# Optimization experiments

Hardware: AMD Instinct MI355X
Metric: run time of the kernel (lower is better)

## Reference

```python
import jax, jax.numpy as jnp
import numpy as np

N, E, IN, H, O = 50000, 800000, 256, 8, 32


def setup_inputs() -> dict:
    key = jax.random.key(0)
    ks = jax.random.split(key, 8)
    feat = jax.random.normal(ks[0], (N, IN), dtype=jnp.float32)
    src = jax.random.randint(ks[1], (E,), 0, N, dtype=jnp.int32)
    dst = jax.random.randint(ks[2], (E,), 0, N, dtype=jnp.int32)
    # Xavier-normal-ish parameter init
    W = jax.random.normal(ks[3], (IN, H * O), dtype=jnp.float32) * (2.0 / (IN + H * O)) ** 0.5
    attn_l = jax.random.normal(ks[4], (H, O), dtype=jnp.float32) * (2.0 / (1 + H * O)) ** 0.5
    attn_r = jax.random.normal(ks[5], (H, O), dtype=jnp.float32) * (2.0 / (1 + H * O)) ** 0.5
    bias = jnp.zeros((H * O,), dtype=jnp.float32)
    return {"feat": feat, "W": W, "attn_l": attn_l, "attn_r": attn_r, "bias": bias, "src": src, "dst": dst}


def reference(feat, W, attn_l, attn_r, bias, src, dst):
    # Linear projection: [N, IN] @ [IN, H*O] -> [N, H, O]
    ft = (feat @ W).reshape(-1, H, O)
    # Additive attention logits per node, per head
    el = jnp.einsum('nho,ho->nh', ft, attn_l)  # [N, H]
    er = jnp.einsum('nho,ho->nh', ft, attn_r)  # [N, H]
    # Edge-wise: e = leaky_relu(el[u] + er[v])
    e = jax.nn.leaky_relu(el[src] + er[dst], negative_slope=0.2)  # [E, H]
    # Segment softmax over incoming edges of each destination node
    emax = jax.ops.segment_max(e, dst, num_segments=N)            # [N, H]
    ee = jnp.exp(e - emax[dst])                                   # [E, H]
    denom = jax.ops.segment_sum(ee, dst, num_segments=N)          # [N, H]
    a = ee / denom[dst]                                           # [E, H]
    # Weighted scatter-sum aggregation: sum_u a_{uv} * ft_u
    msg = ft[src] * a[:, :, None]                                 # [E, H, O]
    rst = jax.ops.segment_sum(msg, dst, num_segments=N)           # [N, H, O]
    rst = rst + bias.reshape(1, H, O)
    return rst
```

## Files before the change

### kernel.cpp

```cpp
#include <hip/hip_runtime.h>

#define N_NODES 50000
#define N_EDGES 800000
#define NPAD    50176
#define SPILL_CAP 8192
#define GEMM_BLOCKS 782
#define BUCKET_BLOCKS 1563

typedef __bf16 bf16x8 __attribute__((ext_vector_type(8)));
typedef float  fx4    __attribute__((ext_vector_type(4)));
typedef unsigned short us8 __attribute__((ext_vector_type(8)));

__device__ __forceinline__ float b2f(unsigned short u) {
    return __uint_as_float(((unsigned)u) << 16);
}
__device__ __forceinline__ unsigned short f2b(float f) {
    unsigned x = __float_as_uint(f);
    return (unsigned short)((x + 0x7FFFu + ((x >> 16) & 1u)) >> 16);
}

__global__ __launch_bounds__(256) void prep_w(
    const float* __restrict__ W,
    unsigned short* __restrict__ Wt,
    int* __restrict__ cursor, int* __restrict__ spill_n) {
    __shared__ float T[64 * 65];
    int b = blockIdx.x, t = threadIdx.x;
    if (b < 16) {
        int bi = b >> 2, bj = b & 3;
        int r = t >> 2, cq = t & 3;
        const float* wp = W + (size_t)(bi * 64 + r) * 256 + bj * 64 + cq * 16;
#pragma unroll
        for (int i = 0; i < 16; ++i) T[r * 65 + cq * 16 + i] = wp[i];
        __syncthreads();
        int n = t >> 2, ks = (t & 3) * 16;
        us8 o0, o1;
#pragma unroll
        for (int i = 0; i < 8; ++i) o0[i] = f2b(T[(ks + i) * 65 + n]);
#pragma unroll
        for (int i = 0; i < 8; ++i) o1[i] = f2b(T[(ks + 8 + i) * 65 + n]);
        unsigned short* op = Wt + (size_t)(bj * 64 + n) * 256 + bi * 64 + ks;
        *reinterpret_cast<us8*>(op) = o0;
        *reinterpret_cast<us8*>(op + 8) = o1;
    } else {
        cursor[(b - 16) * 256 + t] = 0;
        if (b == 16 && t == 0) *spill_n = 0;
    }
}

__global__ __launch_bounds__(512) void gemm_bucket(
    const float* __restrict__ feat,
    const unsigned short* __restrict__ Wt,
    const float* __restrict__ attn_l, const float* __restrict__ attn_r,
    unsigned short* __restrict__ ft,
    float* __restrict__ el, float* __restrict__ er,
    const int* __restrict__ src, const int* __restrict__ dst,
    int* __restrict__ cursor, unsigned short* __restrict__ inedge,
    int* __restrict__ spill_n, int2* __restrict__ spill, int stride) {
    __shared__ unsigned short Alds[64 * 264];
    const int tid = threadIdx.x;

    if (blockIdx.x >= GEMM_BLOCKS) {
        int t = (blockIdx.x - GEMM_BLOCKS) * 512 + tid;
        if (t < N_EDGES) {
            int s = src[t], d = dst[t];
            int idx = atomicAdd(&cursor[d], 1);
            if (idx < stride) {
                inedge[(size_t)d * stride + idx] = (unsigned short)s;
            } else {
                int sp = atomicAdd(spill_n, 1);
                if (sp < SPILL_CAP) spill[sp] = make_int2(s, d);
            }
        }
        return;
    }

    const int lane = tid & 63;
    const int wid  = tid >> 6;
    const int quad = lane >> 4, l15 = lane & 15;
    const int mbase = blockIdx.x * 64;
    const int nbase = wid * 32;

    const unsigned short* wb0 = Wt + (size_t)(nbase + l15) * 256 + quad * 8;
    const unsigned short* wb1 = wb0 + 16 * 256;
    bf16x8 bc0 = *reinterpret_cast<const bf16x8*>(wb0);
    bf16x8 bc1 = *reinterpret_cast<const bf16x8*>(wb1);

    float al0 = attn_l[nbase + l15], al1 = attn_l[nbase + 16 + l15];
    float ar0 = attn_r[nbase + l15], ar1 = attn_r[nbase + 16 + l15];

    fx4 acc[4][2];
#pragma unroll
    for (int i = 0; i < 4; ++i)
#pragma unroll
        for (int j = 0; j < 2; ++j) acc[i][j] = (fx4)0.0f;

    {
        const int srow = tid >> 3, s8 = tid & 7;
        int grow = mbase + srow;
        grow = grow < N_NODES ? grow : N_NODES - 1;
        const float* sp = feat + (size_t)grow * 256;
        unsigned short* sd = &Alds[srow * 264];
#pragma unroll
        for (int ii = 0; ii < 2; ++ii) {
            int c8 = ii * 16 + s8 * 2;
            float4 f0 = *reinterpret_cast<const float4*>(sp + c8 * 8);
            float4 f1 = *reinterpret_cast<const float4*>(sp + c8 * 8 + 4);
            float4 f2 = *reinterpret_cast<const float4*>(sp + c8 * 8 + 8);
            float4 f3 = *reinterpret_cast<const float4*>(sp + c8 * 8 + 12);
            us8 p0, p1;
            p0[0] = f2b(f0.x); p0[1] = f2b(f0.y); p0[2] = f2b(f0.z); p0[3] = f2b(f0.w);
            p0[4] = f2b(f1.x); p0[5] = f2b(f1.y); p0[6] = f2b(f1.z); p0[7] = f2b(f1.w);
            p1[0] = f2b(f2.x); p1[1] = f2b(f2.y); p1[2] = f2b(f2.z); p1[3] = f2b(f2.w);
            p1[4] = f2b(f3.x); p1[5] = f2b(f3.y); p1[6] = f2b(f3.z); p1[7] = f2b(f3.w);
            *reinterpret_cast<us8*>(sd + c8 * 8) = p0;
            *reinterpret_cast<us8*>(sd + c8 * 8 + 8) = p1;
        }
    }
    __syncthreads();

    for (int k0 = 0; k0 < 256; k0 += 32) {
        bf16x8 bn0 = bc0, bn1 = bc1;
        if (k0 < 224) {
            bn0 = *reinterpret_cast<const bf16x8*>(wb0 + k0 + 32);
            bn1 = *reinterpret_cast<const bf16x8*>(wb1 + k0 + 32);
        }
        const int krow = k0 + quad * 8;
        bf16x8 a[4];
#pragma unroll
        for (int mt = 0; mt < 4; ++mt)
            a[mt] = *reinterpret_cast<const bf16x8*>(&Alds[(mt * 16 + l15) * 264 + krow]);
        __builtin_amdgcn_s_setprio(1);
#pragma unroll
        for (int mt = 0; mt < 4; ++mt) {
            acc[mt][0] = __builtin_amdgcn_mfma_f32_16x16x32_bf16(a[mt], bc0, acc[mt][0], 0, 0, 0);
            acc[mt][1] = __builtin_amdgcn_mfma_f32_16x16x32_bf16(a[mt], bc1, acc[mt][1], 0, 0, 0);
        }
        __builtin_amdgcn_s_setprio(0);
        bc0 = bn0; bc1 = bn1;
    }

#pragma unroll
    for (int mt = 0; mt < 4; ++mt) {
#pragma unroll
        for (int r = 0; r < 4; ++r) {
            int row = mbase + mt * 16 + quad * 4 + r;
            float cl = acc[mt][0][r] * al0 + acc[mt][1][r] * al1;
            float cr = acc[mt][0][r] * ar0 + acc[mt][1][r] * ar1;
#pragma unroll
            for (int m = 1; m < 16; m <<= 1) {
                cl += __shfl_xor(cl, m);
                cr += __shfl_xor(cr, m);
            }
            if (row < N_NODES) {
                if (l15 == 0)      el[row * 8 + wid] = cl;
                else if (l15 == 1) er[row * 8 + wid] = cr;
            }
        }
    }
    __syncthreads();

    unsigned short* bw = &Alds[wid * 512];
#pragma unroll
    for (int mt = 0; mt < 4; ++mt) {
#pragma unroll
        for (int r = 0; r < 4; ++r) {
            int rl = quad * 4 + r;
#pragma unroll
            for (int nt = 0; nt < 2; ++nt)
                bw[rl * 32 + nt * 16 + l15] = f2b(acc[mt][nt][r]);
        }
        {
            int rl = lane >> 2;
            int c8 = lane & 3;
            us8 v = *reinterpret_cast<const us8*>(&bw[rl * 32 + c8 * 8]);
            int grow = mbase + mt * 16 + rl;
            if (grow < N_NODES)
                *reinterpret_cast<us8*>(ft + (size_t)grow * 256 + nbase + c8 * 8) = v;
        }
    }
}

__global__ __launch_bounds__(256) void aggregate(
    const unsigned short* __restrict__ ft,
    const float* __restrict__ el, const float* __restrict__ er,
    const int* __restrict__ cursor,
    const unsigned short* __restrict__ inedge,
    const int* __restrict__ spill_n, const int2* __restrict__ spill,
    const float* __restrict__ bias,
    float* __restrict__ out, int stride) {
    int wid = threadIdx.x >> 6, lane = threadIdx.x & 63;
    int v = blockIdx.x * 4 + wid;
    int deg_t = cursor[v];
    int deg = deg_t < stride ? deg_t : stride;
    int half = lane >> 5, l = lane & 31;
    int h = l >> 2;
    int sh = half * 16;
    float erv = er[v * 8 + h];
    const unsigned short* ip = inedge + (size_t)v * stride;
    const us8* ft8 = reinterpret_cast<const us8*>(ft);

    float a[8] = {0.f, 0.f, 0.f, 0.f, 0.f, 0.f, 0.f, 0.f};
    float s = 0.f;
    int j = 0;
    for (; j + 16 <= deg; j += 16) {
        uint4 q0 = *reinterpret_cast<const uint4*>(ip + j);
        uint4 q1 = *reinterpret_cast<const uint4*>(ip + j + 8);
        int u[8];
        u[0] = (q0.x >> sh) & 0xffff; u[1] = (q0.y >> sh) & 0xffff;
        u[2] = (q0.z >> sh) & 0xffff; u[3] = (q0.w >> sh) & 0xffff;
        u[4] = (q1.x >> sh) & 0xffff; u[5] = (q1.y >> sh) & 0xffff;
        u[6] = (q1.z >> sh) & 0xffff; u[7] = (q1.w >> sh) & 0xffff;
        us8 f[8];
#pragma unroll
        for (int t = 0; t < 8; ++t) f[t] = ft8[(size_t)u[t] * 32 + l];
        float ee[8];
#pragma unroll
        for (int t = 0; t < 8; ++t) ee[t] = el[u[t] * 8 + h];
#pragma unroll
        for (int t = 0; t < 8; ++t) {
            float x = ee[t] + erv;
            x = x > 0.f ? x : 0.2f * x;
            float w = __expf(x);
            s += w;
#pragma unroll
            for (int i = 0; i < 8; ++i) a[i] += w * b2f(f[t][i]);
        }
    }
    for (; j + 8 <= deg; j += 8) {
        uint4 q0 = *reinterpret_cast<const uint4*>(ip + j);
        int u[4];
        u[0] = (q0.x >> sh) & 0xffff; u[1] = (q0.y >> sh) & 0xffff;
        u[2] = (q0.z >> sh) & 0xffff; u[3] = (q0.w >> sh) & 0xffff;
        us8 f[4];
#pragma unroll
        for (int t = 0; t < 4; ++t) f[t] = ft8[(size_t)u[t] * 32 + l];
#pragma unroll
        for (int t = 0; t < 4; ++t) {
            float x = el[u[t] * 8 + h] + erv;
            x = x > 0.f ? x : 0.2f * x;
            float w = __expf(x);
            s += w;
#pragma unroll
            for (int i = 0; i < 8; ++i) a[i] += w * b2f(f[t][i]);
        }
    }
    for (; j + 2 <= deg; j += 2) {
        int u = ip[j + half];
        us8 f = ft8[(size_t)u * 32 + l];
        float x = el[u * 8 + h] + erv;
        x = x > 0.f ? x : 0.2f * x;
        float w = __expf(x);
        s += w;
#pragma unroll
        for (int i = 0; i < 8; ++i) a[i] += w * b2f(f[i]);
    }
    if (j < deg && half == 0) {
        int u = ip[j];
        us8 f = ft8[(size_t)u * 32 + l];
        float x = el[u * 8 + h] + erv;
        x = x > 0.f ? x : 0.2f * x;
        float w = __expf(x);
        s += w;
#pragma unroll
        for (int i = 0; i < 8; ++i) a[i] += w * b2f(f[i]);
    }
    if (deg_t > stride) {
        int sn = *spill_n;
        if (sn > SPILL_CAP) sn = SPILL_CAP;
        for (int t = 0; t < sn; ++t) {
            int2 e = spill[t];
            if (e.y == v && half == 0) {
                int u = e.x;
                us8 f = ft8[(size_t)u * 32 + l];
                float x = el[u * 8 + h] + erv;
                x = x > 0.f ? x : 0.2f * x;
                float w = __expf(x);
                s += w;
#pragma unroll
                for (int i = 0; i < 8; ++i) a[i] += w * b2f(f[i]);
            }
        }
    }
#pragma unroll
    for (int i = 0; i < 8; ++i) a[i] += __shfl_xor(a[i], 32);
    s += __shfl_xor(s, 32);
    float inv = deg_t > 0 ? 1.0f / s : 0.f;

    int fi = l * 2 + half;
    float4 bb = reinterpret_cast<const float4*>(bias)[fi];
    int base = half * 4;
    float4 o;
    o.x = a[base + 0] * inv + bb.x;
    o.y = a[base + 1] * inv + bb.y;
    o.z = a[base + 2] * inv + bb.z;
    o.w = a[base + 3] * inv + bb.w;
    reinterpret_cast<float4*>(out)[(size_t)v * 64 + fi] = o;
}

extern "C" void kernel_launch(void* const* d_in, const int* in_sizes, int n_in,
                              void* d_out, int out_size, void* d_ws, size_t ws_size,
                              hipStream_t stream) {
    const float* feat   = (const float*)d_in[0];
    const float* W      = (const float*)d_in[1];
    const float* attn_l = (const float*)d_in[2];
    const float* attn_r = (const float*)d_in[3];
    const float* bias   = (const float*)d_in[4];
    const int* src = (const int*)d_in[5];
    const int* dst = (const int*)d_in[6];
    float* out = (float*)d_out;

    char* ws = (char*)d_ws;
    unsigned short* Wt     = (unsigned short*)(ws + 0);
    unsigned short* ft     = (unsigned short*)(ws + 147456);
    float* el              = (float*)(ws + 25747456);
    float* er              = (float*)(ws + 27347456);
    int* cursor            = (int*)(ws + 28947456);
    int* spill_n           = (int*)(ws + 29148160);
    int2* spill            = (int2*)(ws + 29148224);
    unsigned short* inedge = (unsigned short*)(ws + 29213760);

    size_t avail = ws_size > 29213760ull ? ws_size - 29213760ull : 0;
    int stride = (int)(avail / (2ull * NPAD));
    stride &= ~7;
    if (stride > 64) stride = 64;
    if (stride < 8) stride = 8;

    prep_w<<<212, 256, 0, stream>>>(W, Wt, cursor, spill_n);
    gemm_bucket<<<GEMM_BLOCKS + BUCKET_BLOCKS, 512, 0, stream>>>(
        feat, Wt, attn_l, attn_r, ft, el, er,
        src, dst, cursor, inedge, spill_n, spill, stride);
    aggregate<<<12500, 256, 0, stream>>>(ft, el, er, cursor, inedge,
                                         spill_n, spill, bias, out, stride);
}
```

Baseline: 235.8 us.

## Fold attention vectors into W and compute el/er via extra MFMAs

Precomputes W·attn_l and W·attn_r per head as split hi/lo bf16 matrices in prep_w, so el/er come from extra MFMA tiles in two waves instead of shuffle reductions over the ft accumulators. Edge bucketing now handles four edges per thread with int4 loads, using a quarter of the blocks. The B-operand software prefetch and setprio hints are removed in favor of direct per-iteration loads. The change trades the shuffle-reduction epilogue for extra MFMA work on two waves and slightly changes the rounding of el/er.

```diff
diff --git a/kernel.cpp b/kernel.cpp
--- a/kernel.cpp
+++ b/kernel.cpp
@@ -5,7 +5,7 @@
 #define NPAD    50176
 #define SPILL_CAP 8192
 #define GEMM_BLOCKS 782
-#define BUCKET_BLOCKS 1563
+#define BUCKET_BLOCKS 391
 
 typedef __bf16 bf16x8 __attribute__((ext_vector_type(8)));
 typedef float  fx4    __attribute__((ext_vector_type(4)));
@@ -21,7 +21,9 @@
 
 __global__ __launch_bounds__(256) void prep_w(
     const float* __restrict__ W,
+    const float* __restrict__ attn_l, const float* __restrict__ attn_r,
     unsigned short* __restrict__ Wt,
+    unsigned short* __restrict__ M2t_hi, unsigned short* __restrict__ M2t_lo,
     int* __restrict__ cursor, int* __restrict__ spill_n) {
     __shared__ float T[64 * 65];
     int b = blockIdx.x, t = threadIdx.x;
@@ -41,16 +43,27 @@
         unsigned short* op = Wt + (size_t)(bj * 64 + n) * 256 + bi * 64 + ks;
         *reinterpret_cast<us8*>(op) = o0;
         *reinterpret_cast<us8*>(op + 8) = o1;
+    } else if (b < 32) {
+        int j = b - 16;
+        const float* av = (j < 8) ? (attn_l + j * 32) : (attn_r + (j - 8) * 32);
+        int c0 = (j & 7) * 32;
+        float s = 0.f;
+#pragma unroll
+        for (int o = 0; o < 32; ++o) s += W[t * 256 + c0 + o] * av[o];
+        unsigned short h = f2b(s);
+        M2t_hi[j * 256 + t] = h;
+        M2t_lo[j * 256 + t] = f2b(s - b2f(h));
     } else {
-        cursor[(b - 16) * 256 + t] = 0;
-        if (b == 16 && t == 0) *spill_n = 0;
+        cursor[(b - 32) * 256 + t] = 0;
+        if (b == 32 && t == 0) *spill_n = 0;
     }
 }
 
 __global__ __launch_bounds__(512) void gemm_bucket(
     const float* __restrict__ feat,
     const unsigned short* __restrict__ Wt,
-    const float* __restrict__ attn_l, const float* __restrict__ attn_r,
+    const unsigned short* __restrict__ M2t_hi,
+    const unsigned short* __restrict__ M2t_lo,
     unsigned short* __restrict__ ft,
     float* __restrict__ el, float* __restrict__ er,
     const int* __restrict__ src, const int* __restrict__ dst,
@@ -61,14 +74,20 @@
 
     if (blockIdx.x >= GEMM_BLOCKS) {
         int t = (blockIdx.x - GEMM_BLOCKS) * 512 + tid;
-        if (t < N_EDGES) {
-            int s = src[t], d = dst[t];
-            int idx = atomicAdd(&cursor[d], 1);
-            if (idx < stride) {
-                inedge[(size_t)d * stride + idx] = (unsigned short)s;
-            } else {
-                int sp = atomicAdd(spill_n, 1);
-                if (sp < SPILL_CAP) spill[sp] = make_int2(s, d);
+        if (t < N_EDGES / 4) {
+            int4 s4 = reinterpret_cast<const int4*>(src)[t];
+            int4 d4 = reinterpret_cast<const int4*>(dst)[t];
+            int ss[4] = {s4.x, s4.y, s4.z, s4.w};
+            int dd[4] = {d4.x, d4.y, d4.z, d4.w};
+#pragma unroll
+            for (int i = 0; i < 4; ++i) {
+                int idx = atomicAdd(&cursor[dd[i]], 1);
+                if (idx < stride) {
+                    inedge[(size_t)dd[i] * stride + idx] = (unsigned short)ss[i];
+                } else {
+                    int sp = atomicAdd(spill_n, 1);
+                    if (sp < SPILL_CAP) spill[sp] = make_int2(ss[i], dd[i]);
+                }
             }
         }
         return;
@@ -80,19 +99,20 @@
     const int mbase = blockIdx.x * 64;
     const int nbase = wid * 32;
 
-    const unsigned short* wb0 = Wt + (size_t)(nbase + l15) * 256 + quad * 8;
-    const unsigned short* wb1 = wb0 + 16 * 256;
-    bf16x8 bc0 = *reinterpret_cast<const bf16x8*>(wb0);
-    bf16x8 bc1 = *reinterpret_cast<const bf16x8*>(wb1);
-
-    float al0 = attn_l[nbase + l15], al1 = attn_l[nbase + 16 + l15];
-    float ar0 = attn_r[nbase + l15], ar1 = attn_r[nbase + 16 + l15];
+    const unsigned short* m2base = nullptr;
+    if (wid == 1 || wid == 2) {
+        int jrow = ((wid == 2) ? 8 : 0) + (l15 & 7);
+        m2base = ((l15 < 8) ? M2t_hi : M2t_lo) + jrow * 256;
+    }
 
     fx4 acc[4][2];
-#pragma unroll
-    for (int i = 0; i < 4; ++i)
+    fx4 acce[4];
+#pragma unroll
+    for (int i = 0; i < 4; ++i) {
+        acce[i] = (fx4)0.0f;
 #pragma unroll
         for (int j = 0; j < 2; ++j) acc[i][j] = (fx4)0.0f;
+    }
 
     {
         const int srow = tid >> 3, s8 = tid & 7;
@@ -119,41 +139,39 @@
     __syncthreads();
 
     for (int k0 = 0; k0 < 256; k0 += 32) {
-        bf16x8 bn0 = bc0, bn1 = bc1;
-        if (k0 < 224) {
-            bn0 = *reinterpret_cast<const bf16x8*>(wb0 + k0 + 32);
-            bn1 = *reinterpret_cast<const bf16x8*>(wb1 + k0 + 32);
-        }
         const int krow = k0 + quad * 8;
-        bf16x8 a[4];
+        bf16x8 a[4], b[2];
 #pragma unroll
         for (int mt = 0; mt < 4; ++mt)
             a[mt] = *reinterpret_cast<const bf16x8*>(&Alds[(mt * 16 + l15) * 264 + krow]);
-        __builtin_amdgcn_s_setprio(1);
+#pragma unroll
+        for (int nt = 0; nt < 2; ++nt)
+            b[nt] = *reinterpret_cast<const bf16x8*>(Wt + (nbase + nt * 16 + l15) * 256 + krow);
+#pragma unroll
+        for (int mt = 0; mt < 4; ++mt)
+#pragma unroll
+            for (int nt = 0; nt < 2; ++nt)
+                acc[mt][nt] = __builtin_amdgcn_mfma_f32_16x16x32_bf16(
+                    a[mt], b[nt], acc[mt][nt], 0, 0, 0);
+        if (wid == 1 || wid == 2) {
+            bf16x8 bm = *reinterpret_cast<const bf16x8*>(m2base + krow);
+#pragma unroll
+            for (int mt = 0; mt < 4; ++mt)
+                acce[mt] = __builtin_amdgcn_mfma_f32_16x16x32_bf16(a[mt], bm, acce[mt], 0, 0, 0);
+        }
+    }
+
+    if (wid == 1 || wid == 2) {
+        float* dstp = (wid == 1) ? el : er;
 #pragma unroll
         for (int mt = 0; mt < 4; ++mt) {
-            acc[mt][0] = __builtin_amdgcn_mfma_f32_16x16x32_bf16(a[mt], bc0, acc[mt][0], 0, 0, 0);
-            acc[mt][1] = __builtin_amdgcn_mfma_f32_16x16x32_bf16(a[mt], bc1, acc[mt][1], 0, 0, 0);
-        }
-        __builtin_amdgcn_s_setprio(0);
-        bc0 = bn0; bc1 = bn1;
-    }
-
-#pragma unroll
-    for (int mt = 0; mt < 4; ++mt) {
-#pragma unroll
-        for (int r = 0; r < 4; ++r) {
-            int row = mbase + mt * 16 + quad * 4 + r;
-            float cl = acc[mt][0][r] * al0 + acc[mt][1][r] * al1;
-            float cr = acc[mt][0][r] * ar0 + acc[mt][1][r] * ar1;
-#pragma unroll
-            for (int m = 1; m < 16; m <<= 1) {
-                cl += __shfl_xor(cl, m);
-                cr += __shfl_xor(cr, m);
-            }
-            if (row < N_NODES) {
-                if (l15 == 0)      el[row * 8 + wid] = cl;
-                else if (l15 == 1) er[row * 8 + wid] = cr;
+#pragma unroll
+            for (int r = 0; r < 4; ++r) {
+                int row = mbase + mt * 16 + quad * 4 + r;
+                float c = acce[mt][r];
+                c += __shfl_xor(c, 8);
+                if (row < N_NODES && l15 < 8)
+                    dstp[row * 8 + l15] = c;
             }
         }
     }
@@ -311,6 +329,8 @@
 
     char* ws = (char*)d_ws;
     unsigned short* Wt     = (unsigned short*)(ws + 0);
+    unsigned short* M2t_hi = (unsigned short*)(ws + 131072);
+    unsigned short* M2t_lo = (unsigned short*)(ws + 139264);
     unsigned short* ft     = (unsigned short*)(ws + 147456);
     float* el              = (float*)(ws + 25747456);
     float* er              = (float*)(ws + 27347456);
@@ -325,9 +345,10 @@
     if (stride > 64) stride = 64;
     if (stride < 8) stride = 8;
 
-    prep_w<<<212, 256, 0, stream>>>(W, Wt, cursor, spill_n);
+    prep_w<<<228, 256, 0, stream>>>(W, attn_l, attn_r, Wt, M2t_hi, M2t_lo,
+                                    cursor, spill_n);
     gemm_bucket<<<GEMM_BLOCKS + BUCKET_BLOCKS, 512, 0, stream>>>(
-        feat, Wt, attn_l, attn_r, ft, el, er,
+        feat, Wt, M2t_hi, M2t_lo, ft, el, er,
         src, dst, cursor, inedge, spill_n, spill, stride);
     aggregate<<<12500, 256, 0, stream>>>(ft, el, er, cursor, inedge,
                                          spill_n, spill, bias, out, stride);
```

Result: faster. 226.1 us (-4.1%).
